# Kernel tuning notes

Measured on AMD Instinct MI355X. Metric: run time of the kernel, lower is better.

The kernel has to match this reference:

```python
import jax, jax.numpy as jnp
import numpy as np

N, D, L, OUT, E = 50000, 64, 3, 16, 800000


def setup_inputs() -> dict:
    key = jax.random.key(0)
    ks = jax.random.split(key, 7)
    F = jax.random.normal(ks[0], (N, D), dtype=jnp.float32)
    src = jax.random.randint(ks[1], (E,), 0, N, dtype=jnp.int32)
    dst = jax.random.randint(ks[2], (E,), 0, N, dtype=jnp.int32)
    gcn_w = jax.random.normal(ks[3], (L, D, D), dtype=jnp.float32) / np.float32(np.sqrt(D))
    gcn_b = jnp.zeros((L, D), dtype=jnp.float32)
    fc_w = jax.random.normal(ks[4], (OUT, N * D), dtype=jnp.float32) / np.float32(np.sqrt(N * D))
    fc_b = jnp.zeros((OUT,), dtype=jnp.float32)
    return {"F": F, "src": src, "dst": dst, "gcn_w": gcn_w, "gcn_b": gcn_b,
            "fc_w": fc_w, "fc_b": fc_b}


def reference(F, src, dst, gcn_w, gcn_b, fc_w, fc_b):
    n = F.shape[0]
    # dgl.add_self_loop: append a self edge for every node
    loops = jnp.arange(n, dtype=src.dtype)
    s = jnp.concatenate([src, loops])
    d = jnp.concatenate([dst, loops])
    ones = jnp.ones(s.shape[0], dtype=F.dtype)
    deg_out = jax.ops.segment_sum(ones, s, num_segments=n)  # out-degree of src
    deg_in = jax.ops.segment_sum(ones, d, num_segments=n)   # in-degree of dst
    # self loops guarantee deg >= 1
    norm_src = deg_out ** -0.5
    norm_dst = deg_in ** -0.5
    x = F
    for i in range(gcn_w.shape[0]):
        h = x * norm_src[:, None]                              # [N, D]
        agg = jax.ops.segment_sum(h[s], d, num_segments=n)     # SpMM gather-scatter
        x = (agg * norm_dst[:, None]) @ gcn_w[i] + gcn_b[i]    # GraphConv norm='both'
        x = jax.nn.relu(x)
    flat = jax.nn.relu(x.reshape(-1))                          # Flatten(start_dim=0) + ReLU
    return fc_w @ flat + fc_b                                  # [OUT]
```

## Files before the change

kernel.cpp:

```cpp
#include <hip/hip_runtime.h>
#include <cstdint>

#define Nn 50000
#define Dd 64
#define Ee 800000
#define NBLK 196
#define FC_BLOCKS 512
#define ND4 (Nn*Dd/4)
#define NDTOT ((size_t)Nn * 64)

__device__ __forceinline__ float relu_f(float v){ return v > 0.f ? v : 0.f; }

__device__ __forceinline__ unsigned short f2bf(float f){
    unsigned u = __float_as_uint(f);
    u += 0x7fffu + ((u >> 16) & 1u);
    return (unsigned short)(u >> 16);
}
__device__ __forceinline__ void add_bf8(float* a, uint4 u){
    a[0] += __uint_as_float(u.x << 16);
    a[1] += __uint_as_float(u.x & 0xffff0000u);
    a[2] += __uint_as_float(u.y << 16);
    a[3] += __uint_as_float(u.y & 0xffff0000u);
    a[4] += __uint_as_float(u.z << 16);
    a[5] += __uint_as_float(u.z & 0xffff0000u);
    a[6] += __uint_as_float(u.w << 16);
    a[7] += __uint_as_float(u.w & 0xffff0000u);
}
__device__ __forceinline__ int rowidx(unsigned e, unsigned end, const unsigned* __restrict__ csr){
    unsigned ec = e < (Ee - 1u) ? e : (Ee - 1u);
    int idx = (int)csr[ec];
    return (e < end) ? idx : Nn;
}

__global__ __launch_bounds__(256) void k_degree(const int* __restrict__ src, const int* __restrict__ dst,
                                                unsigned* __restrict__ dout, unsigned* __restrict__ din){
    int e = blockIdx.x * 256 + threadIdx.x;
    if (e < Ee){
        atomicAdd(&dout[src[e]], 1u);
        atomicAdd(&din[dst[e]], 1u);
    }
}

__global__ __launch_bounds__(256) void k_blocksum(const unsigned* __restrict__ din, const unsigned* __restrict__ dout,
                                                  unsigned* __restrict__ bsum,
                                                  float* __restrict__ ns, float* __restrict__ nd){
    __shared__ unsigned s[256];
    int t = threadIdx.x; int i = blockIdx.x * 256 + t;
    unsigned v = (i < Nn) ? din[i] : 0u;
    s[t] = v;
    if (i < Nn){
        ns[i] = rsqrtf((float)(dout[i] + 1u));
        nd[i] = rsqrtf((float)(v + 1u));
    }
    __syncthreads();
    for (int off = 128; off > 0; off >>= 1){ if (t < off) s[t] += s[t + off]; __syncthreads(); }
    if (t == 0) bsum[blockIdx.x] = s[0];
}

__global__ __launch_bounds__(256) void k_scanblocks(const unsigned* __restrict__ bsum, unsigned* __restrict__ boff,
                                                    unsigned* __restrict__ offsets){
    __shared__ unsigned s[256];
    int t = threadIdx.x;
    unsigned v = (t < NBLK) ? bsum[t] : 0u;
    s[t] = v; __syncthreads();
    for (int off = 1; off < 256; off <<= 1){
        unsigned add = (t >= off) ? s[t - off] : 0u;
        __syncthreads();
        s[t] += add;
        __syncthreads();
    }
    boff[t] = s[t] - v;
    if (t == 255) offsets[Nn] = s[255];
}

__global__ __launch_bounds__(256) void k_offsets(const unsigned* __restrict__ din, const unsigned* __restrict__ boff,
                                                 unsigned* __restrict__ offsets, unsigned* __restrict__ cursor){
    __shared__ unsigned s[256];
    int t = threadIdx.x; int i = blockIdx.x * 256 + t;
    unsigned v = (i < Nn) ? din[i] : 0u;
    s[t] = v; __syncthreads();
    for (int off = 1; off < 256; off <<= 1){
        unsigned add = (t >= off) ? s[t - off] : 0u;
        __syncthreads();
        s[t] += add;
        __syncthreads();
    }
    if (i < Nn){
        unsigned val = s[t] - v + boff[blockIdx.x];
        offsets[i] = val;
        cursor[i]  = val;
    }
}

__global__ __launch_bounds__(256) void k_fillcsr(const int* __restrict__ src, const int* __restrict__ dst,
                                                 unsigned* __restrict__ cursor, unsigned* __restrict__ csr){
    int e = blockIdx.x * 256 + threadIdx.x;
    if (e < Ee){
        unsigned pos = atomicAdd(&cursor[dst[e]], 1u);
        csr[pos] = (unsigned)src[e];
    }
}

__global__ __launch_bounds__(256) void k_h0(const float* __restrict__ x, const float* __restrict__ ns,
                                            unsigned short* __restrict__ hA, unsigned short* __restrict__ hB){
    int i = blockIdx.x * 256 + threadIdx.x;
    if (i < ND4){
        const float4* x4 = (const float4*)x;
        float s = ns[i >> 4];
        float4 v = x4[i];
        ushort4 o;
        o.x = f2bf(v.x * s); o.y = f2bf(v.y * s);
        o.z = f2bf(v.z * s); o.w = f2bf(v.w * s);
        ((ushort4*)hA)[i] = o;
    } else {
        int j = i - ND4;
        if (j < 16){
            ushort4 z = make_ushort4(0, 0, 0, 0);
            ((ushort4*)hA)[ND4 + j] = z;
            ((ushort4*)hB)[ND4 + j] = z;
        }
    }
}

__global__ __launch_bounds__(256) void k_gather(const unsigned short* __restrict__ h,
                                                const unsigned* __restrict__ offsets,
                                                const unsigned* __restrict__ csr, const float* __restrict__ nd,
                                                float* __restrict__ agg){
    int v = blockIdx.x * 4 + (threadIdx.x >> 6);
    int lane = threadIdx.x & 63;
    int slot = lane >> 3;
    int sub  = lane & 7;
    const uint4* h16 = (const uint4*)h;

    unsigned beg = offsets[v], end = offsets[v + 1];
    unsigned e0 = beg + slot;

    int i0 = rowidx(e0,      end, csr);
    int i1 = rowidx(e0 + 8,  end, csr);
    int i2 = rowidx(e0 + 16, end, csr);
    int i3 = rowidx(e0 + 24, end, csr);
    uint4 u0 = h16[(size_t)i0 * 8 + sub];
    uint4 u1 = h16[(size_t)i1 * 8 + sub];
    uint4 u2 = h16[(size_t)i2 * 8 + sub];
    uint4 u3 = h16[(size_t)i3 * 8 + sub];

    float acc[8];
    #pragma unroll
    for (int i = 0; i < 8; i++) acc[i] = 0.f;
    if (slot == 0) add_bf8(acc, h16[(size_t)v * 8 + sub]);
    add_bf8(acc, u0);
    add_bf8(acc, u1);
    add_bf8(acc, u2);
    add_bf8(acc, u3);

    for (unsigned e = e0 + 32; e < end; e += 8){
        add_bf8(acc, h16[(size_t)((int)csr[e]) * 8 + sub]);
    }

    #pragma unroll
    for (int i = 0; i < 8; i++) acc[i] += __shfl_xor(acc[i], 8, 64);
    #pragma unroll
    for (int i = 0; i < 8; i++) acc[i] += __shfl_xor(acc[i], 16, 64);
    #pragma unroll
    for (int i = 0; i < 8; i++) acc[i] += __shfl_xor(acc[i], 32, 64);

    if (slot == 0){
        float s = nd[v];
        float4* aggp = (float4*)agg;
        aggp[(size_t)v * 16 + sub * 2 + 0] = make_float4(acc[0] * s, acc[1] * s, acc[2] * s, acc[3] * s);
        aggp[(size_t)v * 16 + sub * 2 + 1] = make_float4(acc[4] * s, acc[5] * s, acc[6] * s, acc[7] * s);
    }
}

__global__ __launch_bounds__(256) void k_gemm(const float* __restrict__ agg, const float* __restrict__ W,
                                              const float* __restrict__ bias, const float* __restrict__ ns,
                                              void* __restrict__ xout, int bf16_prescale_out){
    __shared__ float As[64 * 65];
    __shared__ float Ws[64 * 64];
    int t = threadIdx.x;
    int m_base = blockIdx.x * 64;
    const float4* W4   = (const float4*)W;
    float4* Ws4        = (float4*)Ws;
    const float4* agg4 = (const float4*)agg;
    #pragma unroll
    for (int i = 0; i < 4; i++){
        int g = t + 256 * i;
        Ws4[g] = W4[g];
        int m = g >> 4, q = g & 15;
        int node = m_base + m;
        float4 v = make_float4(0.f, 0.f, 0.f, 0.f);
        if (node < Nn) v = agg4[node * 16 + q];
        float* dp = &As[m * 65 + q * 4];
        dp[0] = v.x; dp[1] = v.y; dp[2] = v.z; dp[3] = v.w;
    }
    __syncthreads();
    int tm = t >> 4, tn = t & 15;
    float acc[4][4];
    #pragma unroll
    for (int i = 0; i < 4; i++)
        #pragma unroll
        for (int j = 0; j < 4; j++) acc[i][j] = 0.f;
    #pragma unroll 4
    for (int k = 0; k < 64; k++){
        float4 w = *(const float4*)&Ws[k * 64 + tn * 4];
        float a[4];
        #pragma unroll
        for (int i = 0; i < 4; i++) a[i] = As[(tm * 4 + i) * 65 + k];
        #pragma unroll
        for (int i = 0; i < 4; i++){
            acc[i][0] += a[i] * w.x;
            acc[i][1] += a[i] * w.y;
            acc[i][2] += a[i] * w.z;
            acc[i][3] += a[i] * w.w;
        }
    }
    float4 b4 = ((const float4*)bias)[tn];
    #pragma unroll
    for (int i = 0; i < 4; i++){
        int node = m_base + tm * 4 + i;
        if (node < Nn){
            float4 r;
            r.x = relu_f(acc[i][0] + b4.x);
            r.y = relu_f(acc[i][1] + b4.y);
            r.z = relu_f(acc[i][2] + b4.z);
            r.w = relu_f(acc[i][3] + b4.w);
            if (bf16_prescale_out){
                float s = ns[node];
                ushort4 o;
                o.x = f2bf(r.x * s); o.y = f2bf(r.y * s);
                o.z = f2bf(r.z * s); o.w = f2bf(r.w * s);
                ((ushort4*)xout)[node * 16 + tn] = o;
            } else {
                ((float4*)xout)[node * 16 + tn] = r;
            }
        }
    }
}

__global__ __launch_bounds__(256) void k_fc(const float* __restrict__ fcw, const float* __restrict__ x,
                                            float* __restrict__ partials){
    int t = threadIdx.x;
    const float4* x4 = (const float4*)x;
    const float4* w4 = (const float4*)fcw;
    float p[16];
    #pragma unroll
    for (int o = 0; o < 16; o++) p[o] = 0.f;
    for (int i = blockIdx.x * 256 + t; i < ND4; i += FC_BLOCKS * 256){
        float4 xv = x4[i];
        #pragma unroll
        for (int o = 0; o < 16; o++){
            float4 wv = w4[(size_t)o * ND4 + i];
            p[o] += wv.x * xv.x + wv.y * xv.y + wv.z * xv.z + wv.w * xv.w;
        }
    }
    #pragma unroll
    for (int o = 0; o < 16; o++){
        for (int off = 32; off > 0; off >>= 1) p[o] += __shfl_down(p[o], off, 64);
    }
    __shared__ float red[4][16];
    int lane = t & 63, wid = t >> 6;
    if (lane == 0){
        #pragma unroll
        for (int o = 0; o < 16; o++) red[wid][o] = p[o];
    }
    __syncthreads();
    if (t < 16) partials[blockIdx.x * 16 + t] = red[0][t] + red[1][t] + red[2][t] + red[3][t];
}

__global__ __launch_bounds__(256) void k_fc2(const float* __restrict__ partials, const float* __restrict__ fcb,
                                             float* __restrict__ out){
    __shared__ float red[256];
    int t = threadIdx.x; int o = t & 15, j0 = t >> 4;
    float s = 0.f;
    for (int j = j0; j < FC_BLOCKS; j += 16) s += partials[j * 16 + o];
    red[t] = s; __syncthreads();
    for (int off = 128; off >= 16; off >>= 1){ if (t < off) red[t] += red[t + off]; __syncthreads(); }
    if (t < 16) out[t] = red[t] + fcb[t];
}

extern "C" void kernel_launch(void* const* d_in, const int* in_sizes, int n_in,
                              void* d_out, int out_size, void* d_ws, size_t ws_size,
                              hipStream_t stream) {
    const float* F     = (const float*)d_in[0];
    const int*   src   = (const int*)d_in[1];
    const int*   dst   = (const int*)d_in[2];
    const float* gcn_w = (const float*)d_in[3];
    const float* gcn_b = (const float*)d_in[4];
    const float* fc_w  = (const float*)d_in[5];
    const float* fc_b  = (const float*)d_in[6];
    float* out = (float*)d_out;

    char* wsp = (char*)d_ws;
    auto alloc = [&](size_t bytes) -> char* {
        char* p = wsp;
        wsp += (bytes + 255) & ~size_t(255);
        return p;
    };
    unsigned* deg      = (unsigned*)alloc(2 * Nn * 4);
    unsigned* deg_out_ = deg;
    unsigned* deg_in_  = deg + Nn;
    unsigned* offsets  = (unsigned*)alloc((Nn + 1) * 4);
    unsigned* cursor   = (unsigned*)alloc(Nn * 4);
    unsigned* bsum     = (unsigned*)alloc(256 * 4);
    unsigned* boff     = (unsigned*)alloc(256 * 4);
    unsigned* csr      = (unsigned*)alloc(Ee * 4);
    float* norm_src    = (float*)alloc(Nn * 4);
    float* norm_dst    = (float*)alloc(Nn * 4);
    float* partials    = (float*)alloc(FC_BLOCKS * 16 * 4);
    unsigned short* hA = (unsigned short*)alloc((NDTOT + 64) * 2);
    unsigned short* hB = (unsigned short*)alloc((NDTOT + 64) * 2);
    float* aggb        = (float*)alloc(NDTOT * 4);
    float* xf          = (float*)alloc(NDTOT * 4);

    hipMemsetAsync(deg, 0, 2 * Nn * 4, stream);

    k_degree<<<Ee / 256, 256, 0, stream>>>(src, dst, deg_out_, deg_in_);
    k_blocksum<<<NBLK, 256, 0, stream>>>(deg_in_, deg_out_, bsum, norm_src, norm_dst);
    k_scanblocks<<<1, 256, 0, stream>>>(bsum, boff, offsets);
    k_offsets<<<NBLK, 256, 0, stream>>>(deg_in_, boff, offsets, cursor);
    k_fillcsr<<<Ee / 256, 256, 0, stream>>>(src, dst, cursor, csr);

    k_h0<<<ND4 / 256 + 1, 256, 0, stream>>>(F, norm_src, hA, hB);

    int nblk_gemm = (Nn + 63) / 64;
    k_gather<<<Nn / 4, 256, 0, stream>>>(hA, offsets, csr, norm_dst, aggb);
    k_gemm<<<nblk_gemm, 256, 0, stream>>>(aggb, gcn_w + 0 * 4096, gcn_b + 0 * 64, norm_src, hB, 1);
    k_gather<<<Nn / 4, 256, 0, stream>>>(hB, offsets, csr, norm_dst, aggb);
    k_gemm<<<nblk_gemm, 256, 0, stream>>>(aggb, gcn_w + 1 * 4096, gcn_b + 1 * 64, norm_src, hA, 1);
    k_gather<<<Nn / 4, 256, 0, stream>>>(hA, offsets, csr, norm_dst, aggb);
    k_gemm<<<nblk_gemm, 256, 0, stream>>>(aggb, gcn_w + 2 * 4096, gcn_b + 2 * 64, norm_src, xf, 0);

    k_fc<<<FC_BLOCKS, 256, 0, stream>>>(fc_w, xf, partials);
    k_fc2<<<1, 256, 0, stream>>>(partials, fc_b, out);
}
```

Baseline: 542.2 us.

## Fuse gather, GEMM and FC per layer; merge scan and CSR/h0 kernels

```diff
diff --git a/kernel.cpp b/kernel.cpp
--- a/kernel.cpp
+++ b/kernel.cpp
@@ -5,7 +5,9 @@
 #define Dd 64
 #define Ee 800000
 #define NBLK 196
-#define FC_BLOCKS 512
+#define EBLK (Ee/256)
+#define LBLK (Nn/16)
+#define H0BLK (ND4/256 + 1)
 #define ND4 (Nn*Dd/4)
 #define NDTOT ((size_t)Nn * 64)
 
@@ -57,26 +59,24 @@
     if (t == 0) bsum[blockIdx.x] = s[0];
 }
 
-__global__ __launch_bounds__(256) void k_scanblocks(const unsigned* __restrict__ bsum, unsigned* __restrict__ boff,
-                                                    unsigned* __restrict__ offsets){
+__global__ __launch_bounds__(256) void k_offsets(const unsigned* __restrict__ din, const unsigned* __restrict__ bsum,
+                                                 unsigned* __restrict__ offsets, unsigned* __restrict__ cursor){
     __shared__ unsigned s[256];
-    int t = threadIdx.x;
-    unsigned v = (t < NBLK) ? bsum[t] : 0u;
-    s[t] = v; __syncthreads();
+    __shared__ unsigned sboff, stot;
+    int t = threadIdx.x; int bid = blockIdx.x;
+    unsigned bv = (t < NBLK) ? bsum[t] : 0u;
+    s[t] = bv; __syncthreads();
     for (int off = 1; off < 256; off <<= 1){
         unsigned add = (t >= off) ? s[t - off] : 0u;
         __syncthreads();
         s[t] += add;
         __syncthreads();
     }
-    boff[t] = s[t] - v;
-    if (t == 255) offsets[Nn] = s[255];
-}
-
-__global__ __launch_bounds__(256) void k_offsets(const unsigned* __restrict__ din, const unsigned* __restrict__ boff,
-                                                 unsigned* __restrict__ offsets, unsigned* __restrict__ cursor){
-    __shared__ unsigned s[256];
-    int t = threadIdx.x; int i = blockIdx.x * 256 + t;
+    if (t == 0)   sboff = (bid > 0) ? s[bid - 1] : 0u;
+    if (t == 255) stot  = s[255];
+    __syncthreads();
+    unsigned boff = sboff;
+    int i = bid * 256 + t;
     unsigned v = (i < Nn) ? din[i] : 0u;
     s[t] = v; __syncthreads();
     for (int off = 1; off < 256; off <<= 1){
@@ -86,185 +86,159 @@
         __syncthreads();
     }
     if (i < Nn){
-        unsigned val = s[t] - v + boff[blockIdx.x];
+        unsigned val = s[t] - v + boff;
         offsets[i] = val;
         cursor[i]  = val;
     }
-}
-
-__global__ __launch_bounds__(256) void k_fillcsr(const int* __restrict__ src, const int* __restrict__ dst,
-                                                 unsigned* __restrict__ cursor, unsigned* __restrict__ csr){
-    int e = blockIdx.x * 256 + threadIdx.x;
-    if (e < Ee){
+    if (bid == 0 && t == 0) offsets[Nn] = stot;
+}
+
+__global__ __launch_bounds__(256) void k_fill_h0(const int* __restrict__ src, const int* __restrict__ dst,
+                                                 unsigned* __restrict__ cursor, unsigned* __restrict__ csr,
+                                                 const float* __restrict__ x, const float* __restrict__ ns,
+                                                 unsigned short* __restrict__ hA, unsigned short* __restrict__ hB){
+    int b = blockIdx.x;
+    if (b < EBLK){
+        int e = b * 256 + threadIdx.x;
         unsigned pos = atomicAdd(&cursor[dst[e]], 1u);
         csr[pos] = (unsigned)src[e];
-    }
-}
-
-__global__ __launch_bounds__(256) void k_h0(const float* __restrict__ x, const float* __restrict__ ns,
-                                            unsigned short* __restrict__ hA, unsigned short* __restrict__ hB){
-    int i = blockIdx.x * 256 + threadIdx.x;
-    if (i < ND4){
-        const float4* x4 = (const float4*)x;
-        float s = ns[i >> 4];
-        float4 v = x4[i];
-        ushort4 o;
-        o.x = f2bf(v.x * s); o.y = f2bf(v.y * s);
-        o.z = f2bf(v.z * s); o.w = f2bf(v.w * s);
-        ((ushort4*)hA)[i] = o;
     } else {
-        int j = i - ND4;
-        if (j < 16){
-            ushort4 z = make_ushort4(0, 0, 0, 0);
-            ((ushort4*)hA)[ND4 + j] = z;
-            ((ushort4*)hB)[ND4 + j] = z;
-        }
-    }
-}
-
-__global__ __launch_bounds__(256) void k_gather(const unsigned short* __restrict__ h,
-                                                const unsigned* __restrict__ offsets,
-                                                const unsigned* __restrict__ csr, const float* __restrict__ nd,
-                                                float* __restrict__ agg){
-    int v = blockIdx.x * 4 + (threadIdx.x >> 6);
-    int lane = threadIdx.x & 63;
-    int slot = lane >> 3;
-    int sub  = lane & 7;
+        int i = (b - EBLK) * 256 + threadIdx.x;
+        if (i < ND4){
+            const float4* x4 = (const float4*)x;
+            float s = ns[i >> 4];
+            float4 v = x4[i];
+            ushort4 o;
+            o.x = f2bf(v.x * s); o.y = f2bf(v.y * s);
+            o.z = f2bf(v.z * s); o.w = f2bf(v.w * s);
+            ((ushort4*)hA)[i] = o;
+        } else {
+            int j = i - ND4;
+            if (j < 16){
+                ushort4 z = make_ushort4(0, 0, 0, 0);
+                ((ushort4*)hA)[ND4 + j] = z;
+                ((ushort4*)hB)[ND4 + j] = z;
+            }
+        }
+    }
+}
+
+__global__ __launch_bounds__(256) void k_layer(const unsigned short* __restrict__ h,
+                                               const unsigned* __restrict__ offsets,
+                                               const unsigned* __restrict__ csr,
+                                               const float* __restrict__ nd,
+                                               const float* __restrict__ W,
+                                               const float* __restrict__ bias,
+                                               const float* __restrict__ ns,
+                                               unsigned short* __restrict__ hout,
+                                               const float* __restrict__ fcw,
+                                               float* __restrict__ partials,
+                                               int fc_mode){
+    __shared__ float Ws[64 * 64];
+    __shared__ float At[64 * 17];
+    __shared__ float red[4][16];
+    int t = threadIdx.x;
+    int nb = blockIdx.x * 16;
+
+    const float4* W4 = (const float4*)W;
+    float4* Ws4 = (float4*)Ws;
+    #pragma unroll
+    for (int i = 0; i < 4; i++) Ws4[t + 256 * i] = W4[t + 256 * i];
+
+    int wv = t >> 6, lane = t & 63;
+    int slot = lane >> 3, sub = lane & 7;
     const uint4* h16 = (const uint4*)h;
 
-    unsigned beg = offsets[v], end = offsets[v + 1];
-    unsigned e0 = beg + slot;
-
-    int i0 = rowidx(e0,      end, csr);
-    int i1 = rowidx(e0 + 8,  end, csr);
-    int i2 = rowidx(e0 + 16, end, csr);
-    int i3 = rowidx(e0 + 24, end, csr);
-    uint4 u0 = h16[(size_t)i0 * 8 + sub];
-    uint4 u1 = h16[(size_t)i1 * 8 + sub];
-    uint4 u2 = h16[(size_t)i2 * 8 + sub];
-    uint4 u3 = h16[(size_t)i3 * 8 + sub];
-
-    float acc[8];
-    #pragma unroll
-    for (int i = 0; i < 8; i++) acc[i] = 0.f;
-    if (slot == 0) add_bf8(acc, h16[(size_t)v * 8 + sub]);
-    add_bf8(acc, u0);
-    add_bf8(acc, u1);
-    add_bf8(acc, u2);
-    add_bf8(acc, u3);
-
-    for (unsigned e = e0 + 32; e < end; e += 8){
-        add_bf8(acc, h16[(size_t)((int)csr[e]) * 8 + sub]);
-    }
-
-    #pragma unroll
-    for (int i = 0; i < 8; i++) acc[i] += __shfl_xor(acc[i], 8, 64);
-    #pragma unroll
-    for (int i = 0; i < 8; i++) acc[i] += __shfl_xor(acc[i], 16, 64);
-    #pragma unroll
-    for (int i = 0; i < 8; i++) acc[i] += __shfl_xor(acc[i], 32, 64);
-
-    if (slot == 0){
-        float s = nd[v];
-        float4* aggp = (float4*)agg;
-        aggp[(size_t)v * 16 + sub * 2 + 0] = make_float4(acc[0] * s, acc[1] * s, acc[2] * s, acc[3] * s);
-        aggp[(size_t)v * 16 + sub * 2 + 1] = make_float4(acc[4] * s, acc[5] * s, acc[6] * s, acc[7] * s);
-    }
-}
-
-__global__ __launch_bounds__(256) void k_gemm(const float* __restrict__ agg, const float* __restrict__ W,
-                                              const float* __restrict__ bias, const float* __restrict__ ns,
-                                              void* __restrict__ xout, int bf16_prescale_out){
-    __shared__ float As[64 * 65];
-    __shared__ float Ws[64 * 64];
-    int t = threadIdx.x;
-    int m_base = blockIdx.x * 64;
-    const float4* W4   = (const float4*)W;
-    float4* Ws4        = (float4*)Ws;
-    const float4* agg4 = (const float4*)agg;
-    #pragma unroll
-    for (int i = 0; i < 4; i++){
-        int g = t + 256 * i;
-        Ws4[g] = W4[g];
-        int m = g >> 4, q = g & 15;
-        int node = m_base + m;
-        float4 v = make_float4(0.f, 0.f, 0.f, 0.f);
-        if (node < Nn) v = agg4[node * 16 + q];
-        float* dp = &As[m * 65 + q * 4];
-        dp[0] = v.x; dp[1] = v.y; dp[2] = v.z; dp[3] = v.w;
+    for (int j = 0; j < 4; j++){
+        int nl = wv * 4 + j;
+        int v  = nb + nl;
+        unsigned beg = 0u, end = 0u;
+        if (v < Nn){ beg = offsets[v]; end = offsets[v + 1]; }
+        unsigned e0 = beg + slot;
+
+        int i0 = rowidx(e0,      end, csr);
+        int i1 = rowidx(e0 + 8,  end, csr);
+        int i2 = rowidx(e0 + 16, end, csr);
+        int i3 = rowidx(e0 + 24, end, csr);
+        uint4 u0 = h16[(size_t)i0 * 8 + sub];
+        uint4 u1 = h16[(size_t)i1 * 8 + sub];
+        uint4 u2 = h16[(size_t)i2 * 8 + sub];
+        uint4 u3 = h16[(size_t)i3 * 8 + sub];
+
+        float acc[8];
+        #pragma unroll
+        for (int i = 0; i < 8; i++) acc[i] = 0.f;
+        if (v < Nn && slot == 0) add_bf8(acc, h16[(size_t)v * 8 + sub]);
+        add_bf8(acc, u0);
+        add_bf8(acc, u1);
+        add_bf8(acc, u2);
+        add_bf8(acc, u3);
+        for (unsigned e = e0 + 32; e < end; e += 8){
+            add_bf8(acc, h16[(size_t)((int)csr[e]) * 8 + sub]);
+        }
+        #pragma unroll
+        for (int i = 0; i < 8; i++) acc[i] += __shfl_xor(acc[i], 8, 64);
+        #pragma unroll
+        for (int i = 0; i < 8; i++) acc[i] += __shfl_xor(acc[i], 16, 64);
+        #pragma unroll
+        for (int i = 0; i < 8; i++) acc[i] += __shfl_xor(acc[i], 32, 64);
+
+        if (slot == 0){
+            float s = (v < Nn) ? nd[v] : 0.f;
+            #pragma unroll
+            for (int i = 0; i < 8; i++) At[(sub * 8 + i) * 17 + nl] = acc[i] * s;
+        }
     }
     __syncthreads();
+
     int tm = t >> 4, tn = t & 15;
-    float acc[4][4];
-    #pragma unroll
-    for (int i = 0; i < 4; i++)
-        #pragma unroll
-        for (int j = 0; j < 4; j++) acc[i][j] = 0.f;
+    float a0 = 0.f, a1 = 0.f, a2 = 0.f, a3 = 0.f;
     #pragma unroll 4
     for (int k = 0; k < 64; k++){
+        float a  = At[k * 17 + tm];
         float4 w = *(const float4*)&Ws[k * 64 + tn * 4];
-        float a[4];
-        #pragma unroll
-        for (int i = 0; i < 4; i++) a[i] = As[(tm * 4 + i) * 65 + k];
-        #pragma unroll
-        for (int i = 0; i < 4; i++){
-            acc[i][0] += a[i] * w.x;
-            acc[i][1] += a[i] * w.y;
-            acc[i][2] += a[i] * w.z;
-            acc[i][3] += a[i] * w.w;
-        }
+        a0 += a * w.x; a1 += a * w.y; a2 += a * w.z; a3 += a * w.w;
     }
     float4 b4 = ((const float4*)bias)[tn];
-    #pragma unroll
-    for (int i = 0; i < 4; i++){
-        int node = m_base + tm * 4 + i;
+    int node = nb + tm;
+    float4 r;
+    r.x = relu_f(a0 + b4.x); r.y = relu_f(a1 + b4.y);
+    r.z = relu_f(a2 + b4.z); r.w = relu_f(a3 + b4.w);
+
+    if (!fc_mode){
         if (node < Nn){
-            float4 r;
-            r.x = relu_f(acc[i][0] + b4.x);
-            r.y = relu_f(acc[i][1] + b4.y);
-            r.z = relu_f(acc[i][2] + b4.z);
-            r.w = relu_f(acc[i][3] + b4.w);
-            if (bf16_prescale_out){
-                float s = ns[node];
-                ushort4 o;
-                o.x = f2bf(r.x * s); o.y = f2bf(r.y * s);
-                o.z = f2bf(r.z * s); o.w = f2bf(r.w * s);
-                ((ushort4*)xout)[node * 16 + tn] = o;
-            } else {
-                ((float4*)xout)[node * 16 + tn] = r;
+            float s = ns[node];
+            ushort4 o4;
+            o4.x = f2bf(r.x * s); o4.y = f2bf(r.y * s);
+            o4.z = f2bf(r.z * s); o4.w = f2bf(r.w * s);
+            ((ushort4*)hout)[(size_t)node * 16 + tn] = o4;
+        }
+    } else {
+        float p[16];
+        const float4* w4 = (const float4*)fcw;
+        size_t base = (size_t)node * 16 + tn;
+        if (node < Nn){
+            #pragma unroll
+            for (int o = 0; o < 16; o++){
+                float4 wv4 = w4[(size_t)o * ND4 + base];
+                p[o] = wv4.x * r.x + wv4.y * r.y + wv4.z * r.z + wv4.w * r.w;
             }
-        }
-    }
-}
-
-__global__ __launch_bounds__(256) void k_fc(const float* __restrict__ fcw, const float* __restrict__ x,
-                                            float* __restrict__ partials){
-    int t = threadIdx.x;
-    const float4* x4 = (const float4*)x;
-    const float4* w4 = (const float4*)fcw;
-    float p[16];
-    #pragma unroll
-    for (int o = 0; o < 16; o++) p[o] = 0.f;
-    for (int i = blockIdx.x * 256 + t; i < ND4; i += FC_BLOCKS * 256){
-        float4 xv = x4[i];
+        } else {
+            #pragma unroll
+            for (int o = 0; o < 16; o++) p[o] = 0.f;
+        }
         #pragma unroll
         for (int o = 0; o < 16; o++){
-            float4 wv = w4[(size_t)o * ND4 + i];
-            p[o] += wv.x * xv.x + wv.y * xv.y + wv.z * xv.z + wv.w * xv.w;
-        }
-    }
-    #pragma unroll
-    for (int o = 0; o < 16; o++){
-        for (int off = 32; off > 0; off >>= 1) p[o] += __shfl_down(p[o], off, 64);
-    }
-    __shared__ float red[4][16];
-    int lane = t & 63, wid = t >> 6;
-    if (lane == 0){
-        #pragma unroll
-        for (int o = 0; o < 16; o++) red[wid][o] = p[o];
-    }
-    __syncthreads();
-    if (t < 16) partials[blockIdx.x * 16 + t] = red[0][t] + red[1][t] + red[2][t] + red[3][t];
+            #pragma unroll
+            for (int off = 32; off > 0; off >>= 1) p[o] += __shfl_down(p[o], off, 64);
+        }
+        if (lane == 0){
+            #pragma unroll
+            for (int o = 0; o < 16; o++) red[wv][o] = p[o];
+        }
+        __syncthreads();
+        if (t < 16) partials[blockIdx.x * 16 + t] = red[0][t] + red[1][t] + red[2][t] + red[3][t];
+    }
 }
 
 __global__ __launch_bounds__(256) void k_fc2(const float* __restrict__ partials, const float* __restrict__ fcb,
@@ -272,7 +246,7 @@
     __shared__ float red[256];
     int t = threadIdx.x; int o = t & 15, j0 = t >> 4;
     float s = 0.f;
-    for (int j = j0; j < FC_BLOCKS; j += 16) s += partials[j * 16 + o];
+    for (int j = j0; j < LBLK; j += 16) s += partials[j * 16 + o];
     red[t] = s; __syncthreads();
     for (int off = 128; off >= 16; off >>= 1){ if (t < off) red[t] += red[t + off]; __syncthreads(); }
     if (t < 16) out[t] = red[t] + fcb[t];
@@ -302,34 +276,26 @@
     unsigned* offsets  = (unsigned*)alloc((Nn + 1) * 4);
     unsigned* cursor   = (unsigned*)alloc(Nn * 4);
     unsigned* bsum     = (unsigned*)alloc(256 * 4);
-    unsigned* boff     = (unsigned*)alloc(256 * 4);
     unsigned* csr      = (unsigned*)alloc(Ee * 4);
     float* norm_src    = (float*)alloc(Nn * 4);
     float* norm_dst    = (float*)alloc(Nn * 4);
-    float* partials    = (float*)alloc(FC_BLOCKS * 16 * 4);
+    float* partials    = (float*)alloc(LBLK * 16 * 4);
     unsigned short* hA = (unsigned short*)alloc((NDTOT + 64) * 2);
     unsigned short* hB = (unsigned short*)alloc((NDTOT + 64) * 2);
-    float* aggb        = (float*)alloc(NDTOT * 4);
-    float* xf          = (float*)alloc(NDTOT * 4);
 
     hipMemsetAsync(deg, 0, 2 * Nn * 4, stream);
 
-    k_degree<<<Ee / 256, 256, 0, stream>>>(src, dst, deg_out_, deg_in_);
+    k_degree <<<EBLK, 256, 0, stream>>>(src, dst, deg_out_, deg_in_);
     k_blocksum<<<NBLK, 256, 0, stream>>>(deg_in_, deg_out_, bsum, norm_src, norm_dst);
-    k_scanblocks<<<1, 256, 0, stream>>>(bsum, boff, offsets);
-    k_offsets<<<NBLK, 256, 0, stream>>>(deg_in_, boff, offsets, cursor);
-    k_fillcsr<<<Ee / 256, 256, 0, stream>>>(src, dst, cursor, csr);
-
-    k_h0<<<ND4 / 256 + 1, 256, 0, stream>>>(F, norm_src, hA, hB);
-
-    int nblk_gemm = (Nn + 63) / 64;
-    k_gather<<<Nn / 4, 256, 0, stream>>>(hA, offsets, csr, norm_dst, aggb);
-    k_gemm<<<nblk_gemm, 256, 0, stream>>>(aggb, gcn_w + 0 * 4096, gcn_b + 0 * 64, norm_src, hB, 1);
-    k_gather<<<Nn / 4, 256, 0, stream>>>(hB, offsets, csr, norm_dst, aggb);
-    k_gemm<<<nblk_gemm, 256, 0, stream>>>(aggb, gcn_w + 1 * 4096, gcn_b + 1 * 64, norm_src, hA, 1);
-    k_gather<<<Nn / 4, 256, 0, stream>>>(hA, offsets, csr, norm_dst, aggb);
-    k_gemm<<<nblk_gemm, 256, 0, stream>>>(aggb, gcn_w + 2 * 4096, gcn_b + 2 * 64, norm_src, xf, 0);
-
-    k_fc<<<FC_BLOCKS, 256, 0, stream>>>(fc_w, xf, partials);
+    k_offsets <<<NBLK, 256, 0, stream>>>(deg_in_, bsum, offsets, cursor);
+    k_fill_h0 <<<EBLK + H0BLK, 256, 0, stream>>>(src, dst, cursor, csr, F, norm_src, hA, hB);
+
+    k_layer<<<LBLK, 256, 0, stream>>>(hA, offsets, csr, norm_dst, gcn_w + 0 * 4096, gcn_b + 0 * 64,
+                                      norm_src, hB, nullptr, nullptr, 0);
+    k_layer<<<LBLK, 256, 0, stream>>>(hB, offsets, csr, norm_dst, gcn_w + 1 * 4096, gcn_b + 1 * 64,
+                                      norm_src, hA, nullptr, nullptr, 0);
+    k_layer<<<LBLK, 256, 0, stream>>>(hA, offsets, csr, norm_dst, gcn_w + 2 * 4096, gcn_b + 2 * 64,
+                                      norm_src, nullptr, fc_w, partials, 1);
+
     k_fc2<<<1, 256, 0, stream>>>(partials, fc_b, out);
 }
```

Result: slower. 565.0 us (+4.2%).
